# Optimization experiments

Measured on AMD Instinct MI355X. Metric: run time of the kernel, lower is better.

The kernel has to match this reference:

```python
import jax, jax.numpy as jnp
import numpy as np

B, T, D, H, F = 4, 2048, 1024, 16, 4096
HD = D // H
EPS = 1e-5


def setup_inputs() -> dict:
    key = jax.random.key(0)
    ks = jax.random.split(key, 10)
    s = lambda fan_in: 1.0 / np.sqrt(fan_in)
    return {
        "x": jax.random.normal(ks[0], (B, T, D), jnp.float32),
        "ln1_g": jnp.ones((D,), jnp.float32),
        "ln1_b": jnp.zeros((D,), jnp.float32),
        "ln2_g": jnp.ones((D,), jnp.float32),
        "ln2_b": jnp.zeros((D,), jnp.float32),
        "Wq": jax.random.normal(ks[1], (H, D, HD), jnp.float32) * s(D),
        "Wk": jax.random.normal(ks[2], (H, D, HD), jnp.float32) * s(D),
        "Wv": jax.random.normal(ks[3], (H, D, HD), jnp.float32) * s(D),
        "Wo": jax.random.normal(ks[4], (D, D), jnp.float32) * s(D),
        "bo": jnp.zeros((D,), jnp.float32),
        "W1": jax.random.normal(ks[5], (D, F), jnp.float32) * s(D),
        "b1": jnp.zeros((F,), jnp.float32),
        "W2": jax.random.normal(ks[6], (F, D), jnp.float32) * s(F),
        "b2": jnp.zeros((D,), jnp.float32),
    }


def _layernorm(x, g, b):
    mu = jnp.mean(x, axis=-1, keepdims=True)
    var = jnp.mean(jnp.square(x - mu), axis=-1, keepdims=True)
    return (x - mu) * jax.lax.rsqrt(var + EPS) * g + b


def reference(x, ln1_g, ln1_b, ln2_g, ln2_b, Wq, Wk, Wv, Wo, bo, W1, b1, W2, b2):
    Bc, Tc, Dc = x.shape
    xn = _layernorm(x, ln1_g, ln1_b)
    # per-head projections (source loops over heads; here batched over h)
    q = jnp.einsum('btd,hdk->bhtk', xn, Wq)
    k = jnp.einsum('btd,hdk->bhtk', xn, Wk)
    v = jnp.einsum('btd,hdk->bhtk', xn, Wv)
    scale = jnp.asarray(Dc, x.dtype) ** -0.5  # C**-0.5 with C = embedding_dim
    scores = jnp.einsum('bhtk,bhsk->bhts', q, k) * scale
    causal = jnp.tril(jnp.ones((Tc, Tc), bool))
    scores = jnp.where(causal, scores, -jnp.inf)
    attn = jax.nn.softmax(scores, axis=-1)
    out = jnp.einsum('bhts,bhsk->bhtk', attn, v)
    out = out.transpose(0, 2, 1, 3).reshape(Bc, Tc, Dc)  # concat heads
    attn_out = out @ Wo + bo
    h = attn_out + x  # residual 1
    hn = _layernorm(h, ln2_g, ln2_b)
    ff = jax.nn.relu(hn @ W1 + b1) @ W2 + b2
    return ff + h  # residual 2
```

## Files before the change

kernel.cpp:

```cpp
#include <hip/hip_runtime.h>
#include <hip/hip_bf16.h>

#define NB 4
#define NT 2048
#define ND 1024
#define NH 16
#define NHD 64
#define NF 4096
#define MTOK (NB*NT)

typedef float f32x4 __attribute__((ext_vector_type(4)));
typedef __bf16 bf16x8 __attribute__((ext_vector_type(8)));
typedef short s16x8 __attribute__((ext_vector_type(8)));
typedef short s16x4v __attribute__((ext_vector_type(4)));
typedef unsigned short ushort_t;

__device__ inline ushort_t f2bf(float f) {
    unsigned int u = __builtin_bit_cast(unsigned int, f);
    unsigned int r = (u + 0x7FFFu + ((u >> 16) & 1u)) >> 16;
    return (ushort_t)r;
}

__device__ __forceinline__ void async_load16(const void* g, void* l) {
    __builtin_amdgcn_global_load_lds(
        (const __attribute__((address_space(1))) void*)g,
        (__attribute__((address_space(3))) void*)l, 16, 0, 0);
}

__device__ __forceinline__ unsigned int cvt_pk_bf16(float lo, float hi) {
    unsigned int r;
    asm("v_cvt_pk_bf16_f32 %0, %1, %2" : "=v"(r) : "v"(lo), "v"(hi));
    return r;
}

__device__ __forceinline__ float exp2_fast(float x) {
    float r;
    asm("v_exp_f32 %0, %1" : "=v"(r) : "v"(x));
    return r;
}

__global__ __launch_bounds__(256)
void transpose_to_bf16(const float* __restrict__ src, ushort_t* __restrict__ dst,
                       int R, int C) {
    __shared__ float tile[32][33];
    int c0 = blockIdx.x * 32, r0 = blockIdx.y * 32;
    #pragma unroll
    for (int i = 0; i < 32; i += 8)
        tile[threadIdx.y + i][threadIdx.x] =
            src[(size_t)(r0 + threadIdx.y + i) * C + c0 + threadIdx.x];
    __syncthreads();
    #pragma unroll
    for (int i = 0; i < 32; i += 8)
        dst[(size_t)(c0 + threadIdx.y + i) * R + r0 + threadIdx.x] =
            f2bf(tile[threadIdx.x][threadIdx.y + i]);
}

__global__ __launch_bounds__(256)
void transpose_qkv_to_bf16(const float* __restrict__ Wq, const float* __restrict__ Wk,
                           const float* __restrict__ Wv, ushort_t* __restrict__ dst) {
    __shared__ float tile[32][33];
    int z = blockIdx.z;
    int w = z >> 4, h = z & 15;
    const float* src = (w == 0 ? Wq : (w == 1 ? Wk : Wv)) + (size_t)h * ND * NHD;
    const float sc = (w == 0) ? 0.03125f * 1.44269504f : 1.0f;
    ushort_t* out = dst + ((size_t)w * ND + h * NHD) * ND;
    int c0 = blockIdx.x * 32, r0 = blockIdx.y * 32;
    #pragma unroll
    for (int i = 0; i < 32; i += 8)
        tile[threadIdx.y + i][threadIdx.x] =
            src[(size_t)(r0 + threadIdx.y + i) * NHD + c0 + threadIdx.x];
    __syncthreads();
    #pragma unroll
    for (int i = 0; i < 32; i += 8)
        out[(size_t)(c0 + threadIdx.y + i) * ND + r0 + threadIdx.x] =
            f2bf(tile[threadIdx.x][threadIdx.y + i] * sc);
}

__global__ __launch_bounds__(256)
void layernorm_to_bf16(const float* __restrict__ x, const float* __restrict__ g,
                       const float* __restrict__ bvec, ushort_t* __restrict__ out) {
    int row = blockIdx.x;
    const float4* xr = (const float4*)(x + (size_t)row * ND);
    float4 v = xr[threadIdx.x];
    float s = v.x + v.y + v.z + v.w;
    float s2 = v.x * v.x + v.y * v.y + v.z * v.z + v.w * v.w;
    #pragma unroll
    for (int o = 32; o >= 1; o >>= 1) {
        s += __shfl_xor(s, o);
        s2 += __shfl_xor(s2, o);
    }
    __shared__ float red[8];
    int wave = threadIdx.x >> 6, lane = threadIdx.x & 63;
    if (lane == 0) { red[wave] = s; red[4 + wave] = s2; }
    __syncthreads();
    float ts = red[0] + red[1] + red[2] + red[3];
    float ts2 = red[4] + red[5] + red[6] + red[7];
    float mu = ts * (1.f / ND);
    float var = ts2 * (1.f / ND) - mu * mu;
    float rs = rsqrtf(var + 1e-5f);
    float4 gv = ((const float4*)g)[threadIdx.x];
    float4 bv = ((const float4*)bvec)[threadIdx.x];
    ushort4 o4;
    o4.x = f2bf((v.x - mu) * rs * gv.x + bv.x);
    o4.y = f2bf((v.y - mu) * rs * gv.y + bv.y);
    o4.z = f2bf((v.z - mu) * rs * gv.z + bv.z);
    o4.w = f2bf((v.w - mu) * rs * gv.w + bv.w);
    ((ushort4*)(out + (size_t)row * ND))[threadIdx.x] = o4;
}

template<bool HAS_BIAS, bool RELU, bool HAS_RES, bool OUT_F32>
__global__ __launch_bounds__(256)
void gemm_bf16(const ushort_t* __restrict__ A, const ushort_t* __restrict__ Bt,
               const float* __restrict__ bias, const float* __restrict__ res,
               void* __restrict__ outp, int M, int N, int K) {
    __shared__ __align__(16) ushort_t As[128 * 64];
    __shared__ __align__(16) ushort_t Bs[128 * 64];
    const int t = threadIdx.x;
    const int wave = t >> 6, lane = t & 63;
    int wid = blockIdx.y * gridDim.x + blockIdx.x;
    const int cpx = (gridDim.x * gridDim.y) >> 3;
    wid = (wid & 7) * cpx + (wid >> 3);
    const int m0 = (wid / gridDim.x) * 128, n0 = (wid % gridDim.x) * 128;
    const int wr = (wave >> 1) * 64, wc = (wave & 1) * 64;
    const int rw = lane >> 3;
    const int ck = lane & 7;
    const int srcCol = (ck ^ rw) * 8;
    f32x4 acc[4][4] = {};

    const ushort_t* Abase = A + (size_t)m0 * K + srcCol;
    const ushort_t* Bbase = Bt + (size_t)n0 * K + srcCol;

    for (int kt = 0; kt < K; kt += 64) {
        __syncthreads();
        #pragma unroll
        for (int c = 0; c < 4; c++) {
            const int rowbase = c * 32 + wave * 8;
            const size_t goff = (size_t)(rowbase + rw) * K + kt;
            async_load16(Abase + goff, As + rowbase * 64);
            async_load16(Bbase + goff, Bs + rowbase * 64);
        }
        __syncthreads();
        #pragma unroll
        for (int ks = 0; ks < 2; ks++) {
            bf16x8 af[4], bfr[4];
            #pragma unroll
            for (int m = 0; m < 4; m++) {
                int row = wr + m * 16 + (lane & 15);
                int a = row * 128 + (ks * 32 + 8 * (lane >> 4)) * 2;
                a ^= ((row & 7) << 4);
                af[m] = *(const bf16x8*)((const char*)As + a);
            }
            #pragma unroll
            for (int n = 0; n < 4; n++) {
                int row = wc + n * 16 + (lane & 15);
                int a = row * 128 + (ks * 32 + 8 * (lane >> 4)) * 2;
                a ^= ((row & 7) << 4);
                bfr[n] = *(const bf16x8*)((const char*)Bs + a);
            }
            #pragma unroll
            for (int m = 0; m < 4; m++)
                #pragma unroll
                for (int n = 0; n < 4; n++)
                    acc[m][n] = __builtin_amdgcn_mfma_f32_16x16x32_bf16(
                        af[m], bfr[n], acc[m][n], 0, 0, 0);
        }
    }

    const int gr0 = m0 + wr + (lane >> 4) * 4;
    const int gc0 = n0 + wc + (lane & 15);
    #pragma unroll
    for (int mf = 0; mf < 4; mf++) {
        #pragma unroll
        for (int nf = 0; nf < 4; nf++) {
            int col = gc0 + nf * 16;
            float bb = 0.f;
            if constexpr (HAS_BIAS) bb = bias[col];
            #pragma unroll
            for (int r = 0; r < 4; r++) {
                int row = gr0 + mf * 16 + r;
                float v = acc[mf][nf][r] + bb;
                if constexpr (RELU) v = fmaxf(v, 0.f);
                if constexpr (HAS_RES) v += res[(size_t)row * N + col];
                if constexpr (OUT_F32)
                    ((float*)outp)[(size_t)row * N + col] = v;
                else
                    ((ushort_t*)outp)[(size_t)row * N + col] = f2bf(v);
            }
        }
    }
}

__global__ __launch_bounds__(256)
void attn_kernel(const ushort_t* __restrict__ qkv, ushort_t* __restrict__ out) {
    __shared__ __align__(16) ushort_t Ks[64 * 64];
    __shared__ __align__(16) ushort_t Vt[64 * 64];
    __shared__ unsigned int Pw[4][32][35];
    const int L = blockIdx.y * gridDim.x + blockIdx.x;
    const int xcd = L & 7, kk = L >> 3;
    const int bh = ((kk & 7) << 3) | xcd;
    const int pairIdx = kk >> 3;
    const int b = bh >> 4, h = bh & 15;
    const int t = threadIdx.x, wave = t >> 6, lane = t & 63;
    const int g = lane >> 4, q16 = lane & 15;
    const size_t base = ((size_t)b * NT) * 3072 + h * NHD;
    const ushort_t* qp_base = qkv + base;
    const ushort_t* kb = qkv + base + 1024;
    const ushort_t* vb = qkv + base + 2048;
    const int krw = lane >> 3, kck = lane & 7;
    const int ksrc = (kck ^ krw) * 8;
    const int vkp = t >> 3, vdg = t & 7;

    for (int half = 0; half < 2; half++) {
        const int qt = half ? (15 - pairIdx) : pairIdx;
        const int q0 = qt * 128;
        const int wq0 = q0 + wave * 32;
        bf16x8 qf[2][2];
        #pragma unroll
        for (int qb2 = 0; qb2 < 2; qb2++) {
            const ushort_t* qp = qp_base + (size_t)(wq0 + 16 * qb2 + q16) * 3072 + 8 * g;
            qf[qb2][0] = *(const bf16x8*)qp;
            qf[qb2][1] = *(const bf16x8*)(qp + 32);
        }
        f32x4 of[2][4] = {};
        float m_run[2] = {-1.0e30f, -1.0e30f};
        float l_run[2] = {0.f, 0.f};
        const int nkv = 2 * qt + 2;

        for (int kv = 0; kv < nkv; ++kv) {
            __syncthreads();
            #pragma unroll
            for (int c = 0; c < 2; c++) {
                const int rowbase = c * 32 + wave * 8;
                async_load16(kb + (size_t)(kv * 64 + rowbase + krw) * 3072 + ksrc,
                             Ks + rowbase * 64);
            }
            {
                const ushort_t* vp = vb + (size_t)(kv * 64 + 2 * vkp) * 3072 + vdg * 8;
                s16x8 v0 = *(const s16x8*)vp;
                s16x8 v1 = *(const s16x8*)(vp + 3072);
                #pragma unroll
                for (int dd = 0; dd < 8; dd++) {
                    int d = vdg * 8 + dd;
                    unsigned int wv = (unsigned int)(ushort_t)v0[dd] |
                                      ((unsigned int)(ushort_t)v1[dd] << 16);
                    int a = (d << 7) + (vkp << 2);
                    a ^= (((d & 7) ^ ((d >> 3) & 7)) << 4);
                    *(unsigned int*)((char*)Vt + a) = wv;
                }
            }
            __syncthreads();

            const int kbase = kv * 64;
            if (kbase > wq0 + 31) continue;

            bf16x8 kf[4][2];
            #pragma unroll
            for (int n = 0; n < 4; n++)
                #pragma unroll
                for (int kd = 0; kd < 2; kd++) {
                    int row = n * 16 + q16;
                    int a = row * 128 + (kd * 64 + 16 * g);
                    a ^= ((row & 7) << 4);
                    kf[n][kd] = *(const bf16x8*)((const char*)Ks + a);
                }

            f32x4 sf[2][4] = {};
            #pragma unroll
            for (int n = 0; n < 4; n++)
                #pragma unroll
                for (int kd = 0; kd < 2; kd++) {
                    sf[0][n] = __builtin_amdgcn_mfma_f32_16x16x32_bf16(
                        kf[n][kd], qf[0][kd], sf[0][n], 0, 0, 0);
                    sf[1][n] = __builtin_amdgcn_mfma_f32_16x16x32_bf16(
                        kf[n][kd], qf[1][kd], sf[1][n], 0, 0, 0);
                }

            #pragma unroll
            for (int qb2 = 0; qb2 < 2; qb2++) {
                const int wqb = wq0 + 16 * qb2 + q16;
                const bool partial = (kbase + 63 > wq0 + 16 * qb2);
                float p[4][4];
                #pragma unroll
                for (int n = 0; n < 4; n++)
                    #pragma unroll
                    for (int r = 0; r < 4; r++) {
                        float v = sf[qb2][n][r];
                        if (partial) {
                            int kg = kbase + n * 16 + 4 * g + r;
                            if (kg > wqb) v = -1.0e30f;
                        }
                        p[n][r] = v;
                    }
                float mx0 = fmaxf(fmaxf(p[0][0], p[0][1]), fmaxf(p[0][2], p[0][3]));
                float mx1 = fmaxf(fmaxf(p[1][0], p[1][1]), fmaxf(p[1][2], p[1][3]));
                float mx2 = fmaxf(fmaxf(p[2][0], p[2][1]), fmaxf(p[2][2], p[2][3]));
                float mx3 = fmaxf(fmaxf(p[3][0], p[3][1]), fmaxf(p[3][2], p[3][3]));
                float mx = fmaxf(fmaxf(mx0, mx1), fmaxf(mx2, mx3));
                mx = fmaxf(mx, __shfl_xor(mx, 16));
                mx = fmaxf(mx, __shfl_xor(mx, 32));
                if (__any(mx > m_run[qb2] + 11.5f)) {
                    float mn = fmaxf(m_run[qb2], mx);
                    float corr = exp2_fast(m_run[qb2] - mn);
                    m_run[qb2] = mn;
                    l_run[qb2] *= corr;
                    #pragma unroll
                    for (int nf = 0; nf < 4; nf++) {
                        f32x4 o4 = of[qb2][nf];
                        o4[0] *= corr; o4[1] *= corr; o4[2] *= corr; o4[3] *= corr;
                        of[qb2][nf] = o4;
                    }
                }
                float ps = 0.f;
                #pragma unroll
                for (int n = 0; n < 4; n++)
                    #pragma unroll
                    for (int r = 0; r < 4; r++) {
                        p[n][r] = exp2_fast(p[n][r] - m_run[qb2]);
                        ps += p[n][r];
                    }
                ps += __shfl_xor(ps, 16);
                ps += __shfl_xor(ps, 32);
                l_run[qb2] += ps;
                unsigned int* pr = &Pw[wave][16 * qb2 + q16][0];
                #pragma unroll
                for (int n = 0; n < 4; n++) {
                    pr[8 * n + 2 * g + 0] = cvt_pk_bf16(p[n][0], p[n][1]);
                    pr[8 * n + 2 * g + 1] = cvt_pk_bf16(p[n][2], p[n][3]);
                }
            }

            #pragma unroll
            for (int kbk = 0; kbk < 2; kbk++) {
                bf16x8 pfr[2];
                #pragma unroll
                for (int qb2 = 0; qb2 < 2; qb2++) {
                    const unsigned int* pr = &Pw[wave][16 * qb2 + q16][0];
                    uint4 pu;
                    pu.x = pr[16 * kbk + 4 * g + 0];
                    pu.y = pr[16 * kbk + 4 * g + 1];
                    pu.z = pr[16 * kbk + 4 * g + 2];
                    pu.w = pr[16 * kbk + 4 * g + 3];
                    pfr[qb2] = __builtin_bit_cast(bf16x8, pu);
                }
                #pragma unroll
                for (int nf = 0; nf < 4; nf++) {
                    const int d = nf * 16 + q16;
                    int a = (d << 7) + (kbk * 64 + 16 * g);
                    a ^= (((d & 7) ^ ((d >> 3) & 7)) << 4);
                    bf16x8 vf = *(const bf16x8*)((const char*)Vt + a);
                    of[0][nf] = __builtin_amdgcn_mfma_f32_16x16x32_bf16(
                        vf, pfr[0], of[0][nf], 0, 0, 0);
                    of[1][nf] = __builtin_amdgcn_mfma_f32_16x16x32_bf16(
                        vf, pfr[1], of[1][nf], 0, 0, 0);
                }
            }
        }

        #pragma unroll
        for (int qb2 = 0; qb2 < 2; qb2++) {
            float rl = 1.f / l_run[qb2];
            const size_t orow = (size_t)b * NT + q0 + wave * 32 + 16 * qb2 + q16;
            #pragma unroll
            for (int nf = 0; nf < 4; nf++) {
                ushort4 o4;
                o4.x = f2bf(of[qb2][nf][0] * rl);
                o4.y = f2bf(of[qb2][nf][1] * rl);
                o4.z = f2bf(of[qb2][nf][2] * rl);
                o4.w = f2bf(of[qb2][nf][3] * rl);
                *(ushort4*)(out + orow * ND + h * NHD + nf * 16 + 4 * g) = o4;
            }
        }
    }
}

extern "C" void kernel_launch(void* const* d_in, const int* in_sizes, int n_in,
                              void* d_out, int out_size, void* d_ws, size_t ws_size,
                              hipStream_t stream) {
    const float* x     = (const float*)d_in[0];
    const float* ln1_g = (const float*)d_in[1];
    const float* ln1_b = (const float*)d_in[2];
    const float* ln2_g = (const float*)d_in[3];
    const float* ln2_b = (const float*)d_in[4];
    const float* Wq    = (const float*)d_in[5];
    const float* Wk    = (const float*)d_in[6];
    const float* Wv    = (const float*)d_in[7];
    const float* Wo    = (const float*)d_in[8];
    const float* bo    = (const float*)d_in[9];
    const float* W1    = (const float*)d_in[10];
    const float* b1    = (const float*)d_in[11];
    const float* W2    = (const float*)d_in[12];
    const float* b2    = (const float*)d_in[13];
    float* outp = (float*)d_out;

    char* w = (char*)d_ws;
    ushort_t* Wqkv_t = (ushort_t*)(w);
    ushort_t* Wo_t   = (ushort_t*)(w + 6291456);
    ushort_t* W1_t   = (ushort_t*)(w + 8388608);
    ushort_t* W2_t   = (ushort_t*)(w + 16777216);
    ushort_t* xn     = (ushort_t*)(w + 25165824);
    ushort_t* qkv    = (ushort_t*)(w + 41943040);
    ushort_t* attn_o = qkv + (size_t)MTOK * 3072;
    ushort_t* ff1    = qkv;
    float*    hbuf   = (float*)(w + 41943040 + 67108864);

    dim3 tb(32, 8);
    transpose_qkv_to_bf16<<<dim3(2, 32, 48), tb, 0, stream>>>(Wq, Wk, Wv, Wqkv_t);
    transpose_to_bf16<<<dim3(32, 32), tb, 0, stream>>>(Wo, Wo_t, 1024, 1024);
    transpose_to_bf16<<<dim3(128, 32), tb, 0, stream>>>(W1, W1_t, 1024, 4096);
    transpose_to_bf16<<<dim3(32, 128), tb, 0, stream>>>(W2, W2_t, 4096, 1024);

    layernorm_to_bf16<<<MTOK, 256, 0, stream>>>(x, ln1_g, ln1_b, xn);

    gemm_bf16<false, false, false, false><<<dim3(24, 64), 256, 0, stream>>>(
        xn, Wqkv_t, nullptr, nullptr, qkv, MTOK, 3072, 1024);

    attn_kernel<<<dim3(8, 64), 256, 0, stream>>>(qkv, attn_o);

    gemm_bf16<true, false, true, true><<<dim3(8, 64), 256, 0, stream>>>(
        attn_o, Wo_t, bo, x, hbuf, MTOK, 1024, 1024);

    layernorm_to_bf16<<<MTOK, 256, 0, stream>>>(hbuf, ln2_g, ln2_b, xn);

    gemm_bf16<true, true, false, false><<<dim3(32, 64), 256, 0, stream>>>(
        xn, W1_t, b1, nullptr, ff1, MTOK, NF, 1024);

    gemm_bf16<true, false, true, true><<<dim3(8, 64), 256, 0, stream>>>(
        ff1, W2_t, b2, hbuf, outp, MTOK, 1024, NF);
}
```

Baseline: 398.9 us.

## Replace 128x128 GEMM with double-buffered 256-row tile, 512-thread pipelined kernel

Replaces the single-buffered 128x128 bf16 GEMM with a 512-thread kernel using 256xBN tiles (BN=128 or 256), double-buffered LDS, and async global-to-LDS prefetch of the next A tile and the B tile two steps ahead. Waits use explicit vmcnt counts and raw s_barrier, and MFMA sections are wrapped in s_setprio. The goal is to hide global load latency behind MFMA work and raise arithmetic intensity per block. The cost is more LDS and registers per block, fewer blocks in each grid, and hand-counted vmcnt waits that must match the number of loads in flight.

```diff
diff --git a/kernel.cpp b/kernel.cpp
--- a/kernel.cpp
+++ b/kernel.cpp
@@ -12,7 +12,6 @@
 typedef float f32x4 __attribute__((ext_vector_type(4)));
 typedef __bf16 bf16x8 __attribute__((ext_vector_type(8)));
 typedef short s16x8 __attribute__((ext_vector_type(8)));
-typedef short s16x4v __attribute__((ext_vector_type(4)));
 typedef unsigned short ushort_t;
 
 __device__ inline ushort_t f2bf(float f) {
@@ -108,77 +107,121 @@
     ((ushort4*)(out + (size_t)row * ND))[threadIdx.x] = o4;
 }
 
-template<bool HAS_BIAS, bool RELU, bool HAS_RES, bool OUT_F32>
-__global__ __launch_bounds__(256)
-void gemm_bf16(const ushort_t* __restrict__ A, const ushort_t* __restrict__ Bt,
-               const float* __restrict__ bias, const float* __restrict__ res,
-               void* __restrict__ outp, int M, int N, int K) {
-    __shared__ __align__(16) ushort_t As[128 * 64];
-    __shared__ __align__(16) ushort_t Bs[128 * 64];
+template<int BN, bool HAS_BIAS, bool RELU, bool HAS_RES, bool OUT_F32>
+__global__ __launch_bounds__(512, 2)
+void gemm256(const ushort_t* __restrict__ A, const ushort_t* __restrict__ Bt,
+             const float* __restrict__ bias, const float* __restrict__ res,
+             void* __restrict__ outp, int M, int N, int K) {
+    constexpr int NFR = BN / 64;
+    constexpr int BISS = BN / 64;
+    __shared__ __align__(16) ushort_t As[2][256 * 64];
+    __shared__ __align__(16) ushort_t Bs[2][BN * 64];
     const int t = threadIdx.x;
     const int wave = t >> 6, lane = t & 63;
+    const int wm = wave >> 2, wn = wave & 3;
+    const int g = lane >> 4, l16 = lane & 15;
     int wid = blockIdx.y * gridDim.x + blockIdx.x;
     const int cpx = (gridDim.x * gridDim.y) >> 3;
     wid = (wid & 7) * cpx + (wid >> 3);
-    const int m0 = (wid / gridDim.x) * 128, n0 = (wid % gridDim.x) * 128;
-    const int wr = (wave >> 1) * 64, wc = (wave & 1) * 64;
-    const int rw = lane >> 3;
-    const int ck = lane & 7;
-    const int srcCol = (ck ^ rw) * 8;
-    f32x4 acc[4][4] = {};
-
+    const int m0 = (wid / gridDim.x) * 256;
+    const int n0 = (wid % gridDim.x) * BN;
+    const int lrow8 = lane >> 3;
+    const int srcCol = ((lane & 7) ^ lrow8) * 8;
     const ushort_t* Abase = A + (size_t)m0 * K + srcCol;
     const ushort_t* Bbase = Bt + (size_t)n0 * K + srcCol;
-
-    for (int kt = 0; kt < K; kt += 64) {
-        __syncthreads();
-        #pragma unroll
-        for (int c = 0; c < 4; c++) {
-            const int rowbase = c * 32 + wave * 8;
-            const size_t goff = (size_t)(rowbase + rw) * K + kt;
-            async_load16(Abase + goff, As + rowbase * 64);
-            async_load16(Bbase + goff, Bs + rowbase * 64);
-        }
-        __syncthreads();
-        #pragma unroll
-        for (int ks = 0; ks < 2; ks++) {
-            bf16x8 af[4], bfr[4];
-            #pragma unroll
-            for (int m = 0; m < 4; m++) {
-                int row = wr + m * 16 + (lane & 15);
-                int a = row * 128 + (ks * 32 + 8 * (lane >> 4)) * 2;
-                a ^= ((row & 7) << 4);
-                af[m] = *(const bf16x8*)((const char*)As + a);
-            }
-            #pragma unroll
-            for (int n = 0; n < 4; n++) {
-                int row = wc + n * 16 + (lane & 15);
-                int a = row * 128 + (ks * 32 + 8 * (lane >> 4)) * 2;
-                a ^= ((row & 7) << 4);
-                bfr[n] = *(const bf16x8*)((const char*)Bs + a);
-            }
-            #pragma unroll
-            for (int m = 0; m < 4; m++)
-                #pragma unroll
-                for (int n = 0; n < 4; n++)
-                    acc[m][n] = __builtin_amdgcn_mfma_f32_16x16x32_bf16(
-                        af[m], bfr[n], acc[m][n], 0, 0, 0);
+    const int NKT = K >> 6;
+
+    f32x4 acc[8][NFR] = {};
+
+    auto stageA = [&](int kt, int slot) {
+        #pragma unroll
+        for (int j = 0; j < 4; j++) {
+            const int rowbase = j * 64 + wave * 8;
+            async_load16(Abase + (size_t)(rowbase + lrow8) * K + kt * 64,
+                         &As[slot][rowbase * 64]);
+        }
+    };
+    auto stageB = [&](int kt, int slot) {
+        #pragma unroll
+        for (int j = 0; j < BISS; j++) {
+            const int rowbase = j * 64 + wave * 8;
+            async_load16(Bbase + (size_t)(rowbase + lrow8) * K + kt * 64,
+                         &Bs[slot][rowbase * 64]);
+        }
+    };
+
+    stageA(0, 0);
+    stageB(0, 0);
+    stageB(1, 1);
+
+    for (int kt = 0; kt < NKT; ++kt) {
+        const int cur = kt & 1;
+        if (kt == NKT - 1) {
+            asm volatile("s_waitcnt vmcnt(0)" ::: "memory");
+        } else if constexpr (BN == 256) {
+            asm volatile("s_waitcnt vmcnt(4)" ::: "memory");
+        } else {
+            asm volatile("s_waitcnt vmcnt(2)" ::: "memory");
+        }
+        __builtin_amdgcn_s_barrier();
+
+        const ushort_t* as = As[cur];
+        const ushort_t* bs = Bs[cur];
+
+        bf16x8 bfr[NFR][2];
+        #pragma unroll
+        for (int nf = 0; nf < NFR; nf++)
+            #pragma unroll
+            for (int ks = 0; ks < 2; ks++) {
+                const int row = wn * (BN / 4) + nf * 16 + l16;
+                int a = row * 128 + ks * 64 + 16 * g;
+                a ^= (row & 7) << 4;
+                bfr[nf][ks] = *(const bf16x8*)((const char*)bs + a);
+            }
+        if (kt + 1 < NKT) stageA(kt + 1, cur ^ 1);
+
+        #pragma unroll
+        for (int q = 0; q < 4; q++) {
+            if (q == 2) {
+                __builtin_amdgcn_s_barrier();
+                if (kt + 2 < NKT) stageB(kt + 2, cur);
+            }
+            bf16x8 af[2][2];
+            #pragma unroll
+            for (int mi2 = 0; mi2 < 2; mi2++)
+                #pragma unroll
+                for (int ks = 0; ks < 2; ks++) {
+                    const int row = wm * 128 + (q * 2 + mi2) * 16 + l16;
+                    int a = row * 128 + ks * 64 + 16 * g;
+                    a ^= (row & 7) << 4;
+                    af[mi2][ks] = *(const bf16x8*)((const char*)as + a);
+                }
+            __builtin_amdgcn_s_setprio(1);
+            #pragma unroll
+            for (int mi2 = 0; mi2 < 2; mi2++)
+                #pragma unroll
+                for (int nf = 0; nf < NFR; nf++)
+                    #pragma unroll
+                    for (int ks = 0; ks < 2; ks++)
+                        acc[q * 2 + mi2][nf] = __builtin_amdgcn_mfma_f32_16x16x32_bf16(
+                            af[mi2][ks], bfr[nf][ks], acc[q * 2 + mi2][nf], 0, 0, 0);
+            __builtin_amdgcn_s_setprio(0);
         }
     }
 
-    const int gr0 = m0 + wr + (lane >> 4) * 4;
-    const int gc0 = n0 + wc + (lane & 15);
-    #pragma unroll
-    for (int mf = 0; mf < 4; mf++) {
-        #pragma unroll
-        for (int nf = 0; nf < 4; nf++) {
-            int col = gc0 + nf * 16;
+    const int gr0 = m0 + wm * 128 + g * 4;
+    const int gc0 = n0 + wn * (BN / 4) + l16;
+    #pragma unroll
+    for (int mi = 0; mi < 8; mi++) {
+        #pragma unroll
+        for (int nf = 0; nf < NFR; nf++) {
+            const int col = gc0 + nf * 16;
             float bb = 0.f;
             if constexpr (HAS_BIAS) bb = bias[col];
             #pragma unroll
             for (int r = 0; r < 4; r++) {
-                int row = gr0 + mf * 16 + r;
-                float v = acc[mf][nf][r] + bb;
+                const int row = gr0 + mi * 16 + r;
+                float v = acc[mi][nf][r] + bb;
                 if constexpr (RELU) v = fmaxf(v, 0.f);
                 if constexpr (HAS_RES) v += res[(size_t)row * N + col];
                 if constexpr (OUT_F32)
@@ -411,19 +454,19 @@
 
     layernorm_to_bf16<<<MTOK, 256, 0, stream>>>(x, ln1_g, ln1_b, xn);
 
-    gemm_bf16<false, false, false, false><<<dim3(24, 64), 256, 0, stream>>>(
+    gemm256<128, false, false, false, false><<<dim3(24, 32), 512, 0, stream>>>(
         xn, Wqkv_t, nullptr, nullptr, qkv, MTOK, 3072, 1024);
 
     attn_kernel<<<dim3(8, 64), 256, 0, stream>>>(qkv, attn_o);
 
-    gemm_bf16<true, false, true, true><<<dim3(8, 64), 256, 0, stream>>>(
+    gemm256<128, true, false, true, true><<<dim3(8, 32), 512, 0, stream>>>(
         attn_o, Wo_t, bo, x, hbuf, MTOK, 1024, 1024);
 
     layernorm_to_bf16<<<MTOK, 256, 0, stream>>>(hbuf, ln2_g, ln2_b, xn);
 
-    gemm_bf16<true, true, false, false><<<dim3(32, 64), 256, 0, stream>>>(
+    gemm256<256, true, true, false, false><<<dim3(16, 32), 512, 0, stream>>>(
         xn, W1_t, b1, nullptr, ff1, MTOK, NF, 1024);
 
-    gemm_bf16<true, false, true, true><<<dim3(8, 64), 256, 0, stream>>>(
+    gemm256<128, true, false, true, true><<<dim3(8, 32), 512, 0, stream>>>(
         ff1, W2_t, b2, hbuf, outp, MTOK, 1024, NF);
 }
```

Result: faster. 388.9 us (-2.5%).
